# Optimization experiments

Hardware: AMD Instinct MI355X
Metric: run time of the kernel (lower is better)

The kernel has to match this reference:

```python
import jax, jax.numpy as jnp
import numpy as np

M = 4096   # nodes per layer (also number of input nodes)
L = 32     # internal layers
K = 64     # in-degree of each internal node


def setup_inputs() -> dict:
    key = jax.random.key(0)
    k_x, k_wi, k_bi, k_w, k_b, k_g = jax.random.split(key, 6)
    x = jax.random.normal(k_x, (M, 1), dtype=jnp.float32)
    w_in = jax.random.normal(k_wi, (M, 1), dtype=jnp.float32)
    b_in = jax.random.normal(k_bi, (M,), dtype=jnp.float32)
    # scale internal weights so sigmoid(K-term dot) is not fully saturated
    w = jax.random.normal(k_w, (L, M, K), dtype=jnp.float32) * 0.05
    b = jax.random.normal(k_b, (L, M), dtype=jnp.float32)
    # predecessor indices into the previous layer's value vector
    igraf = jax.random.randint(k_g, (L, M, K), 0, M, dtype=jnp.int32)
    return {"x": x, "w_in": w_in, "b_in": b_in, "w": w, "b": b, "igraf": igraf}


def reference(x, w_in, b_in, w, b, igraf):
    # input nodes: relu(Linear(1,1)) applied to each scalar input, vectorized
    v = jax.nn.relu(w_in[:, 0] * x[:, 0] + b_in)          # [M]
    # internal nodes, layer by layer (topological order):
    # each node gathers K predecessor values and applies sigmoid(Linear(K,1))
    for l in range(L):
        g = v[igraf[l]]                                   # [M, K] irregular gather
        v = jax.nn.sigmoid(jnp.einsum('mk,mk->m', w[l], g) + b[l])
    # original returns values[n_nodes - 1] (shape [1])
    return v[-1:]
```

## Files before the change

kernel.cpp:

```cpp
#include <hip/hip_runtime.h>

#define M 4096
#define L 32
#define K 64
#define NBLK 64
#define BLOCK 256
#define NPB 64
#define EPT 16
#define MK (M * K)
#define POISON 0xAAAAAAAAu

__global__ __launch_bounds__(BLOCK)
void net_kernel(const float* __restrict__ x,
                const float* __restrict__ w_in,
                const float* __restrict__ b_in,
                const float* __restrict__ w,
                const float* __restrict__ b,
                const int* __restrict__ igraf,
                float* __restrict__ out,
                unsigned int* __restrict__ buf)
{
    __shared__ float sv[2][M];

    const int tid   = threadIdx.x;
    const int blk   = blockIdx.x;
    const int node  = blk * NPB + (tid >> 2);
    const int chunk = tid & 3;
    const bool pub  = (chunk == 0);
    const bool lastblk = (blk == NBLK - 1);

    const size_t fbase = (size_t)node * K + (size_t)chunk * EPT;

    float4 wv[4]; int4 iv[4]; float breg = 0.0f;
    {
        const float4* wp = (const float4*)(w + fbase);
        const int4*   ip = (const int4*)(igraf + fbase);
        wv[0] = wp[0]; wv[1] = wp[1]; wv[2] = wp[2]; wv[3] = wp[3];
        iv[0] = ip[0]; iv[1] = ip[1]; iv[2] = ip[2]; iv[3] = ip[3];
        if (pub) breg = b[node];
    }

    #pragma unroll
    for (int j = 0; j < 4; ++j) {
        const int idx = tid + j * BLOCK;
        const float4 x4 = ((const float4*)x)[idx];
        const float4 wi = ((const float4*)w_in)[idx];
        const float4 bi = ((const float4*)b_in)[idx];
        float4 r;
        r.x = fmaxf(fmaf(wi.x, x4.x, bi.x), 0.0f);
        r.y = fmaxf(fmaf(wi.y, x4.y, bi.y), 0.0f);
        r.z = fmaxf(fmaf(wi.z, x4.z, bi.z), 0.0f);
        r.w = fmaxf(fmaf(wi.w, x4.w, bi.w), 0.0f);
        ((float4*)sv[0])[idx] = r;
    }
    __syncthreads();

    for (int t = 0; t < L; ++t) {
        const float* svc = sv[t & 1];
        float p = 0.0f;
        #pragma unroll
        for (int q = 0; q < 4; ++q) {
            p = fmaf(wv[q].x, svc[iv[q].x], p);
            p = fmaf(wv[q].y, svc[iv[q].y], p);
            p = fmaf(wv[q].z, svc[iv[q].z], p);
            p = fmaf(wv[q].w, svc[iv[q].w], p);
        }
        p += __shfl_xor(p, 1, 64);
        p += __shfl_xor(p, 2, 64);

        float val = 0.0f;
        if (pub) val = 1.0f / (1.0f + __expf(-(p + breg)));

        if (t == L - 1) {
            if (tid == 252) out[0] = val;
            break;
        }

        if (pub) {
            __hip_atomic_store(&buf[(size_t)t * M + node],
                               __float_as_uint(val),
                               __ATOMIC_RELAXED, __HIP_MEMORY_SCOPE_AGENT);
        }

        if (t == L - 2 && !lastblk) return;

        {
            const size_t nb = (size_t)(t + 1) * MK + fbase;
            const float4* wp = (const float4*)(w + nb);
            const int4*   ip = (const int4*)(igraf + nb);
            wv[0] = wp[0]; wv[1] = wp[1]; wv[2] = wp[2]; wv[3] = wp[3];
            iv[0] = ip[0]; iv[1] = ip[1]; iv[2] = ip[2]; iv[3] = ip[3];
            if (pub) breg = b[(t + 1) * M + node];
        }
        __builtin_amdgcn_sched_barrier(0);

        const unsigned int* src = buf + (size_t)t * M;
        unsigned int vals[16];
        #pragma unroll
        for (int j = 0; j < 16; ++j)
            vals[j] = __hip_atomic_load(&src[tid + j * BLOCK],
                                        __ATOMIC_RELAXED,
                                        __HIP_MEMORY_SCOPE_AGENT);

        for (;;) {
            bool ok = true;
            #pragma unroll
            for (int j = 0; j < 16; ++j) {
                if (vals[j] == POISON) {
                    ok = false;
                    vals[j] = __hip_atomic_load(&src[tid + j * BLOCK],
                                                __ATOMIC_RELAXED,
                                                __HIP_MEMORY_SCOPE_AGENT);
                }
            }
            if (ok) break;
        }

        float* svn = sv[(t + 1) & 1];
        #pragma unroll
        for (int j = 0; j < 16; ++j)
            svn[tid + j * BLOCK] = __uint_as_float(vals[j]);
        __syncthreads();
    }
}

extern "C" void kernel_launch(void* const* d_in, const int* in_sizes, int n_in,
                              void* d_out, int out_size, void* d_ws, size_t ws_size,
                              hipStream_t stream) {
    const float* x     = (const float*)d_in[0];
    const float* w_in  = (const float*)d_in[1];
    const float* b_in  = (const float*)d_in[2];
    const float* wt    = (const float*)d_in[3];
    const float* b     = (const float*)d_in[4];
    const int*   igraf = (const int*)d_in[5];
    float*       out   = (float*)d_out;

    unsigned int* buf = (unsigned int*)d_ws;

    hipLaunchKernelGGL(net_kernel, dim3(NBLK), dim3(BLOCK), 0, stream,
                       x, w_in, b_in, wt, b, igraf, out, buf);
    (void)in_sizes; (void)n_in; (void)out_size; (void)ws_size;
}
```

Measured before the change: 156.8 us.

## Pin all worker blocks to one XCC and poll with L2-local loads

The grid grows to 512 blocks. Each block reads its hardware XCC id and publishes it in a registry, then all blocks agree on the most populated XCC, and only the first 64 blocks on that XCC do the work. Keeping the inter-block handoffs inside one XCC's L2 lets the polling loop use plain sc0 loads instead of device-scope atomics, with a fallback to atomic loads after a few spins. This relies on the workspace being poisoned, on hardware XCC id semantics, and on at least 64 blocks landing on one XCC, and it adds registry setup at kernel start.

```diff
diff --git a/kernel.cpp b/kernel.cpp
--- a/kernel.cpp
+++ b/kernel.cpp
@@ -1,14 +1,18 @@
 #include <hip/hip_runtime.h>
+#include <stdint.h>
 
 #define M 4096
 #define L 32
 #define K 64
-#define NBLK 64
+#define NWORK 64
+#define GRID 512
 #define BLOCK 256
 #define NPB 64
 #define EPT 16
+#define ENT 16
 #define MK (M * K)
 #define POISON 0xAAAAAAAAu
+#define FAST_SPINS 16
 
 __global__ __launch_bounds__(BLOCK)
 void net_kernel(const float* __restrict__ x,
@@ -21,13 +25,62 @@
                 unsigned int* __restrict__ buf)
 {
     __shared__ float sv[2][M];
-
-    const int tid   = threadIdx.x;
-    const int blk   = blockIdx.x;
-    const int node  = blk * NPB + (tid >> 2);
-    const int chunk = tid & 3;
-    const bool pub  = (chunk == 0);
-    const bool lastblk = (blk == NBLK - 1);
+    __shared__ unsigned sreg[GRID];
+    __shared__ int counts[8];
+    __shared__ int starget;
+    __shared__ int srankc;
+
+    const int tid = threadIdx.x;
+    const int blk = blockIdx.x;
+
+    unsigned myxcc;
+    asm volatile("s_getreg_b32 %0, hwreg(HW_REG_XCC_ID)" : "=s"(myxcc));
+    myxcc &= 7u;
+
+    unsigned int* reg = buf + (size_t)(L - 1) * M;
+    if (tid == 0) {
+        __hip_atomic_store(&reg[blk], myxcc,
+                           __ATOMIC_RELAXED, __HIP_MEMORY_SCOPE_AGENT);
+        srankc = 0;
+    }
+    if (tid < 8) counts[tid] = 0;
+
+    #pragma unroll
+    for (int j = 0; j < GRID / BLOCK; ++j) {
+        const int i = tid + j * BLOCK;
+        unsigned v;
+        do {
+            v = __hip_atomic_load(&reg[i], __ATOMIC_RELAXED,
+                                  __HIP_MEMORY_SCOPE_AGENT);
+        } while (v == POISON);
+        sreg[i] = v & 7u;
+    }
+    __syncthreads();
+    #pragma unroll
+    for (int j = 0; j < GRID / BLOCK; ++j)
+        atomicAdd(&counts[sreg[tid + j * BLOCK]], 1);
+    __syncthreads();
+    if (tid == 0) {
+        int best = 0;
+        for (int k2 = 1; k2 < 8; ++k2)
+            if (counts[k2] > counts[best]) best = k2;
+        starget = best;
+    }
+    __syncthreads();
+    const unsigned target = (unsigned)starget;
+    #pragma unroll
+    for (int j = 0; j < GRID / BLOCK; ++j) {
+        const int i = tid + j * BLOCK;
+        if (i < blk && sreg[i] == target) atomicAdd(&srankc, 1);
+    }
+    __syncthreads();
+    const int rank = srankc;
+    if (sreg[blk] != target || rank >= NWORK) return;
+
+    const int  node  = rank * NPB + (tid >> 2);
+    const int  chunk = tid & 3;
+    const bool pub   = (chunk == 0);
+    const bool lastrank = (rank == NWORK - 1);
 
     const size_t fbase = (size_t)node * K + (size_t)chunk * EPT;
 
@@ -77,12 +130,15 @@
         }
 
         if (pub) {
-            __hip_atomic_store(&buf[(size_t)t * M + node],
-                               __float_as_uint(val),
+            unsigned int* dst = buf + (size_t)t * M + node;
+            const unsigned bits = __float_as_uint(val);
+            asm volatile("global_store_dword %0, %1, off"
+                         :: "v"(dst), "v"(bits) : "memory");
+            __hip_atomic_store(dst, bits,
                                __ATOMIC_RELAXED, __HIP_MEMORY_SCOPE_AGENT);
         }
 
-        if (t == L - 2 && !lastblk) return;
+        if (t == L - 2 && !lastrank) return;
 
         {
             const size_t nb = (size_t)(t + 1) * MK + fbase;
@@ -94,31 +150,49 @@
         }
         __builtin_amdgcn_sched_barrier(0);
 
-        const unsigned int* src = buf + (size_t)t * M;
-        unsigned int vals[16];
+        const unsigned int* srcrow = buf + (size_t)t * M;
+        unsigned int vals[ENT];
         #pragma unroll
-        for (int j = 0; j < 16; ++j)
-            vals[j] = __hip_atomic_load(&src[tid + j * BLOCK],
-                                        __ATOMIC_RELAXED,
-                                        __HIP_MEMORY_SCOPE_AGENT);
-
+        for (int j = 0; j < ENT; ++j) {
+            const unsigned int* ap = srcrow + tid + j * BLOCK;
+            asm volatile("global_load_dword %0, %1, off sc0"
+                         : "=&v"(vals[j]) : "v"(ap));
+        }
+        asm volatile("s_waitcnt vmcnt(0)" ::: "memory");
+        __builtin_amdgcn_sched_barrier(0);
+
+        int spins = 0;
         for (;;) {
-            bool ok = true;
+            unsigned stale = 0u;
             #pragma unroll
-            for (int j = 0; j < 16; ++j) {
-                if (vals[j] == POISON) {
-                    ok = false;
-                    vals[j] = __hip_atomic_load(&src[tid + j * BLOCK],
-                                                __ATOMIC_RELAXED,
-                                                __HIP_MEMORY_SCOPE_AGENT);
+            for (int j = 0; j < ENT; ++j)
+                stale |= ((unsigned)(vals[j] == POISON)) << j;
+            if (!stale) break;
+            ++spins;
+            if (spins <= FAST_SPINS) {
+                #pragma unroll
+                for (int j = 0; j < ENT; ++j) {
+                    if (stale & (1u << j)) {
+                        const unsigned int* ap = srcrow + tid + j * BLOCK;
+                        asm volatile("global_load_dword %0, %1, off sc0"
+                                     : "=&v"(vals[j]) : "v"(ap));
+                    }
                 }
+                asm volatile("s_waitcnt vmcnt(0)" ::: "memory");
+                __builtin_amdgcn_sched_barrier(0);
+            } else {
+                #pragma unroll
+                for (int j = 0; j < ENT; ++j)
+                    if (stale & (1u << j))
+                        vals[j] = __hip_atomic_load(&srcrow[tid + j * BLOCK],
+                                                    __ATOMIC_RELAXED,
+                                                    __HIP_MEMORY_SCOPE_AGENT);
             }
-            if (ok) break;
         }
 
         float* svn = sv[(t + 1) & 1];
         #pragma unroll
-        for (int j = 0; j < 16; ++j)
+        for (int j = 0; j < ENT; ++j)
             svn[tid + j * BLOCK] = __uint_as_float(vals[j]);
         __syncthreads();
     }
@@ -137,7 +211,7 @@
 
     unsigned int* buf = (unsigned int*)d_ws;
 
-    hipLaunchKernelGGL(net_kernel, dim3(NBLK), dim3(BLOCK), 0, stream,
+    hipLaunchKernelGGL(net_kernel, dim3(GRID), dim3(BLOCK), 0, stream,
                        x, w_in, b_in, wt, b, igraf, out, buf);
     (void)in_sizes; (void)n_in; (void)out_size; (void)ws_size;
 }
```

New measurement: 510.8 us. 226% more time.
